# Kernel optimization log

Measured on AMD Instinct MI355X. Metric: run time of the kernel, lower is better.

Reference implementation:

```python
import jax, jax.numpy as jnp
import numpy as np

N = 50000   # nodes
E = 200000  # edges (avg degree ~4, pose-graph-like sparsity)
F_IN = 512
NEG_SLOPE = 0.01  # F.leaky_relu default


def _softmax_aggr(src_feat, dst, num_nodes):
    # torch_geometric SoftmaxAggregation(t=1): per-destination, per-feature
    # alpha = softmax(x_j), out = sum_j alpha * x_j
    m = jax.ops.segment_max(src_feat, dst, num_segments=num_nodes)  # [N,F]
    m = jnp.where(jnp.isfinite(m), m, 0.0)  # empty segments -> -inf guard
    e = jnp.exp(src_feat - m[dst])                                   # [E,F]
    denom = jax.ops.segment_sum(e, dst, num_segments=num_nodes)      # [N,F]
    num = jax.ops.segment_sum(e * src_feat, dst, num_segments=num_nodes)
    return num / jnp.maximum(denom, 1e-16)  # 0 for isolated nodes


def setup_inputs() -> dict:
    key = jax.random.key(0)
    ks = jax.random.split(key, 9)
    inp = {
        "x": jax.random.normal(ks[0], (N, F_IN), dtype=jnp.float32),
        "W1_rel": jax.random.normal(ks[1], (513, 256), dtype=jnp.float32) * 0.04,
        "b1_rel": jnp.zeros((256,), dtype=jnp.float32),
        "W1_root": jax.random.normal(ks[2], (513, 256), dtype=jnp.float32) * 0.04,
        "W2_rel": jax.random.normal(ks[3], (257, 64), dtype=jnp.float32) * 0.06,
        "b2_rel": jnp.zeros((64,), dtype=jnp.float32),
        "W2_root": jax.random.normal(ks[4], (257, 64), dtype=jnp.float32) * 0.06,
        "Wp": jax.random.normal(ks[5], (65, 3), dtype=jnp.float32) * 0.1,
        "bp": jnp.zeros((3,), dtype=jnp.float32),
        "Wr": jax.random.normal(ks[6], (65, 4), dtype=jnp.float32) * 0.1,
        "br": jnp.zeros((4,), dtype=jnp.float32),
        "edge_index": jax.random.randint(ks[7], (2, E), 0, N, dtype=jnp.int64),
    }
    return inp


def reference(x, W1_rel, b1_rel, W1_root, W2_rel, b2_rel, W2_root,
              Wp, bp, Wr, br, edge_index):
    src, dst = edge_index[0], edge_index[1]
    node_index = jnp.arange(x.shape[0], dtype=x.dtype)[:, None]  # [N,1]

    # dropout is identity in eval mode
    h = jnp.concatenate([x, node_index], axis=1)  # [N,513]

    # GraphConv(513,256, aggr='softmax'): lin_rel(softmax_aggr(x_j)) + lin_root(x)
    agg1 = _softmax_aggr(h[src], dst, x.shape[0])               # [N,513]
    h = agg1 @ W1_rel + b1_rel + h @ W1_root                     # [N,256]
    h = jnp.where(h >= 0, h, NEG_SLOPE * h)

    h = jnp.concatenate([h, node_index], axis=1)  # [N,257]

    # GraphConv(257,64) default aggr='add'
    agg2 = jax.ops.segment_sum(h[src], dst, num_segments=x.shape[0])  # [N,257]
    h = agg2 @ W2_rel + b2_rel + h @ W2_root                           # [N,64]
    h = jnp.where(h >= 0, h, NEG_SLOPE * h)

    h = jnp.concatenate([h, node_index], axis=1)  # [N,65]

    position = h @ Wp + bp                         # [N,3]
    rotation = h @ Wr + br                         # [N,4]
    norm = jnp.linalg.norm(rotation, axis=1, keepdims=True)
    rotation = rotation / jnp.maximum(norm, 1e-12)  # F.normalize

    return jnp.concatenate([position, rotation], axis=1)  # [N,7]
```

## Files before the change

### kernel.cpp

```cpp
#include <hip/hip_runtime.h>

#define NNODES 50000
#define NEDGES 200000
#define NSCANB ((NNODES + 255) / 256)

typedef short  bf16x8 __attribute__((ext_vector_type(8)));
typedef float  f32x4  __attribute__((ext_vector_type(4)));
typedef unsigned int u32x4 __attribute__((ext_vector_type(4)));

__device__ __forceinline__ unsigned short f2bf(float f) {
    union { float f; unsigned int u; } c; c.f = f;
    unsigned int r = c.u + 0x7fffu + ((c.u >> 16) & 1u);
    return (unsigned short)(r >> 16);
}
__device__ __forceinline__ float bf2f(unsigned short h) {
    union { unsigned int u; float f; } c; c.u = ((unsigned int)h) << 16;
    return c.f;
}
__device__ __forceinline__ float bflo(unsigned int v) {
    union { unsigned int u; float f; } c; c.u = v << 16;
    return c.f;
}
__device__ __forceinline__ float bfhi(unsigned int v) {
    union { unsigned int u; float f; } c; c.u = v & 0xffff0000u;
    return c.f;
}

#define PREP_B1 (256 * 1024)
#define PREP_B2 (64 * 512)
#define PREP_XC (NNODES * 64)
__global__ __launch_bounds__(256) void k_prepcount(const float* __restrict__ x,
                                                   const float* __restrict__ W1_rel,
                                                   const float* __restrict__ W1_root,
                                                   const float* __restrict__ W2_rel,
                                                   const float* __restrict__ W2_root,
                                                   const int* __restrict__ ei,
                                                   int* __restrict__ deg,
                                                   unsigned short* __restrict__ Bt1,
                                                   unsigned short* __restrict__ Bt2,
                                                   unsigned short* __restrict__ xb) {
    const int gtid = blockIdx.x * 256 + threadIdx.x;
    const int GS = gridDim.x * 256;
    for (int e = gtid; e < NEDGES; e += GS) atomicAdd(&deg[ei[NEDGES + e]], 1);
    for (int i = gtid; i < PREP_B1; i += GS) {
        int n = i >> 10, k = i & 1023;
        float v = (k < 512) ? W1_rel[k * 256 + n] : W1_root[(k - 512) * 256 + n];
        Bt1[i] = f2bf(v);
    }
    for (int i = gtid; i < PREP_B2; i += GS) {
        int n = i >> 9, k = i & 511;
        float v = (k < 256) ? W2_rel[k * 64 + n] : W2_root[(k - 256) * 64 + n];
        Bt2[i] = f2bf(v);
    }
    for (int i = gtid; i < PREP_XC; i += GS) {
        int n = i >> 6, c8 = (i & 63) * 8;
        const float* xp = x + (size_t)n * 512 + c8;
        float4 a = *(const float4*)xp;
        float4 bb = *(const float4*)(xp + 4);
        unsigned short o[8];
        o[0] = f2bf(a.x); o[1] = f2bf(a.y); o[2] = f2bf(a.z); o[3] = f2bf(a.w);
        o[4] = f2bf(bb.x); o[5] = f2bf(bb.y); o[6] = f2bf(bb.z); o[7] = f2bf(bb.w);
        *(u32x4*)(xb + (size_t)n * 512 + c8) = *(const u32x4*)o;
    }
}

__global__ __launch_bounds__(256) void k_scanA(const int* __restrict__ deg,
                                               int* __restrict__ rs,
                                               int* __restrict__ partials) {
    __shared__ int sm[256];
    int t = threadIdx.x, i = blockIdx.x * 256 + t;
    int v = (i < NNODES) ? deg[i] : 0;
    sm[t] = v;
    __syncthreads();
#pragma unroll
    for (int off = 1; off < 256; off <<= 1) {
        int u = (t >= off) ? sm[t - off] : 0;
        __syncthreads();
        sm[t] += u;
        __syncthreads();
    }
    if (i < NNODES) rs[i] = sm[t] - v;
    if (t == 255) partials[blockIdx.x] = sm[255];
}

__global__ __launch_bounds__(256) void k_scanC2(int* __restrict__ rs,
                                                const int* __restrict__ partials,
                                                int* __restrict__ cursor) {
    __shared__ int sm[256];
    int t = threadIdx.x, b = blockIdx.x;
    sm[t] = (t < b && t < NSCANB) ? partials[t] : 0;
    __syncthreads();
#pragma unroll
    for (int off = 128; off; off >>= 1) {
        if (t < off) sm[t] += sm[t + off];
        __syncthreads();
    }
    int off0 = sm[0];
    int i = b * 256 + t;
    if (i < NNODES) {
        int rv = rs[i] + off0;
        rs[i] = rv;
        cursor[i] = rv;
    }
    if (i == 0) rs[NNODES] = NEDGES;
}

__global__ void k_scatter(const int* __restrict__ ei, int* __restrict__ cursor,
                          int* __restrict__ srcs) {
    int e = blockIdx.x * 256 + threadIdx.x;
    if (e < NEDGES) {
        int d = ei[NEDGES + e];
        int p = atomicAdd(&cursor[d], 1);
        srcs[p] = ei[e];
    }
}

__global__ __launch_bounds__(256) void k_agg1(const unsigned short* __restrict__ xb,
                                              const int* __restrict__ rs,
                                              const int* __restrict__ srcs,
                                              unsigned short* __restrict__ AggBuf) {
    int wv = threadIdx.x >> 6;
    int lane = threadIdx.x & 63;
    int n = blockIdx.x * 4 + wv;
    int e0 = rs[n], e1 = rs[n + 1];
    float nu[8], de[8];
#pragma unroll
    for (int j = 0; j < 8; ++j) { nu[j] = 0.f; de[j] = 0.f; }
    int e = e0;
    for (; e + 1 < e1; e += 2) {
        int s0 = srcs[e], s1 = srcs[e + 1];
        u32x4 r0 = *(const u32x4*)(xb + (size_t)s0 * 512 + lane * 8);
        u32x4 r1 = *(const u32x4*)(xb + (size_t)s1 * 512 + lane * 8);
#pragma unroll
        for (int p = 0; p < 4; ++p) {
            float v0 = bflo(r0[p]), v1 = bfhi(r0[p]);
            float E0 = __expf(v0), E1 = __expf(v1);
            de[2 * p] += E0; nu[2 * p] += E0 * v0;
            de[2 * p + 1] += E1; nu[2 * p + 1] += E1 * v1;
        }
#pragma unroll
        for (int p = 0; p < 4; ++p) {
            float v0 = bflo(r1[p]), v1 = bfhi(r1[p]);
            float E0 = __expf(v0), E1 = __expf(v1);
            de[2 * p] += E0; nu[2 * p] += E0 * v0;
            de[2 * p + 1] += E1; nu[2 * p + 1] += E1 * v1;
        }
    }
    if (e < e1) {
        int s0 = srcs[e];
        u32x4 r0 = *(const u32x4*)(xb + (size_t)s0 * 512 + lane * 8);
#pragma unroll
        for (int p = 0; p < 4; ++p) {
            float v0 = bflo(r0[p]), v1 = bfhi(r0[p]);
            float E0 = __expf(v0), E1 = __expf(v1);
            de[2 * p] += E0; nu[2 * p] += E0 * v0;
            de[2 * p + 1] += E1; nu[2 * p + 1] += E1 * v1;
        }
    }
    unsigned short o[8];
#pragma unroll
    for (int j = 0; j < 8; ++j) o[j] = f2bf(nu[j] / fmaxf(de[j], 1e-16f));
    *(u32x4*)(AggBuf + (size_t)n * 512 + lane * 8) = *(const u32x4*)o;
}

__global__ __launch_bounds__(256) void k_agg2(const int* __restrict__ rs,
                                              const int* __restrict__ srcs,
                                              const unsigned short* __restrict__ H1,
                                              unsigned short* __restrict__ Seg) {
    int wv = threadIdx.x >> 6;
    int lane = threadIdx.x & 63;
    int n = blockIdx.x * 4 + wv;
    int e0 = rs[n], e1 = rs[n + 1];
    float a[4] = {0.f, 0.f, 0.f, 0.f};
    int e = e0;
    for (; e + 1 < e1; e += 2) {
        int s0 = srcs[e], s1 = srcs[e + 1];
        uint2 r0 = *(const uint2*)(H1 + (size_t)s0 * 256 + lane * 4);
        uint2 r1 = *(const uint2*)(H1 + (size_t)s1 * 256 + lane * 4);
        a[0] += bflo(r0.x) + bflo(r1.x);
        a[1] += bfhi(r0.x) + bfhi(r1.x);
        a[2] += bflo(r0.y) + bflo(r1.y);
        a[3] += bfhi(r0.y) + bfhi(r1.y);
    }
    if (e < e1) {
        uint2 r0 = *(const uint2*)(H1 + (size_t)srcs[e] * 256 + lane * 4);
        a[0] += bflo(r0.x); a[1] += bfhi(r0.x);
        a[2] += bflo(r0.y); a[3] += bfhi(r0.y);
    }
    uint2 o;
    o.x = (unsigned int)f2bf(a[0]) | ((unsigned int)f2bf(a[1]) << 16);
    o.y = (unsigned int)f2bf(a[2]) | ((unsigned int)f2bf(a[3]) << 16);
    *(uint2*)(Seg + (size_t)n * 256 + lane * 4) = o;
}

__global__ __launch_bounds__(256, 5) void k_gemm1(const unsigned short* __restrict__ A1,
                                                  const unsigned short* __restrict__ A2,
                                                  const unsigned short* __restrict__ Bt,
                                                  const int* __restrict__ rs,
                                                  const int* __restrict__ srcs,
                                                  const float* __restrict__ r1,
                                                  const float* __restrict__ r2,
                                                  const float* __restrict__ bias,
                                                  unsigned short* __restrict__ outp) {
    constexpr int BM = 64, BN = 128, BK = 64;
    __shared__ __align__(16) unsigned short As[BM * BK];
    __shared__ __align__(16) unsigned short Bs[BN * BK];
    __shared__ float s1t[BM];

    const int tid = threadIdx.x;
    const int w = tid >> 6;
    const int lane = tid & 63;
    const int lm = lane & 15;
    const int quad = lane >> 4;
    const int wr = w >> 1;
    const int wc = w & 1;
    const int rowbase = blockIdx.y * BM;
    const int colbase = blockIdx.x * BN;
    const int wrow = wr * 32;
    const int wcol = wc * 64;

    const int rsub = lane >> 3;
    const int csw = (lane & 7) ^ rsub;

    f32x4 acc[2][4];
#pragma unroll
    for (int mi = 0; mi < 2; ++mi)
#pragma unroll
        for (int ni = 0; ni < 4; ++ni) acc[mi][ni] = (f32x4){0.f, 0.f, 0.f, 0.f};

    for (int kt = 0; kt < 1024; kt += BK) {
        const unsigned short* Ab = (kt < 512) ? A1 : A2;
        int kof = (kt < 512) ? kt : kt - 512;
#pragma unroll
        for (int l = 0; l < 2; ++l) {
            int r = w * 16 + l * 8;
            int gr = rowbase + r + rsub;
            if (gr >= NNODES) gr = NNODES - 1;
            const unsigned short* gp = Ab + (size_t)gr * 512 + kof + csw * 8;
            __builtin_amdgcn_global_load_lds(
                (const __attribute__((address_space(1))) void*)gp,
                (__attribute__((address_space(3))) void*)(As + r * BK), 16, 0, 0);
        }
#pragma unroll
        for (int l = 0; l < 4; ++l) {
            int r = w * 32 + l * 8;
            const unsigned short* gp = Bt + (size_t)(colbase + r + rsub) * 1024 + kt + csw * 8;
            __builtin_amdgcn_global_load_lds(
                (const __attribute__((address_space(1))) void*)gp,
                (__attribute__((address_space(3))) void*)(Bs + r * BK), 16, 0, 0);
        }
        __syncthreads();
#pragma unroll
        for (int kk = 0; kk < BK; kk += 32) {
            const int kidx = (kk >> 3) + quad;
            const int phys = kidx ^ (lm & 7);
            bf16x8 af[2], bfr[4];
#pragma unroll
            for (int mi = 0; mi < 2; ++mi)
                af[mi] = __builtin_bit_cast(bf16x8,
                    *(const u32x4*)(As + (wrow + mi * 16 + lm) * BK + phys * 8));
#pragma unroll
            for (int ni = 0; ni < 4; ++ni)
                bfr[ni] = __builtin_bit_cast(bf16x8,
                    *(const u32x4*)(Bs + (wcol + ni * 16 + lm) * BK + phys * 8));
#pragma unroll
            for (int mi = 0; mi < 2; ++mi)
#pragma unroll
                for (int ni = 0; ni < 4; ++ni)
                    acc[mi][ni] = __builtin_amdgcn_mfma_f32_16x16x32_bf16(
                        af[mi], bfr[ni], acc[mi][ni], 0, 0, 0);
        }
        __syncthreads();
    }

    if (tid < BM) {
        int grow = rowbase + tid;
        float r_ = 0.f;
        if (grow < NNODES) {
            int e0 = rs[grow], e1 = rs[grow + 1];
            float m = -INFINITY, d = 0.f, q = 0.f;
            for (int e = e0; e < e1; ++e) {
                float v = (float)srcs[e];
                float nm = fmaxf(m, v);
                float sc = __expf(m - nm), ee = __expf(v - nm);
                d = d * sc + ee;
                q = q * sc + ee * v;
                m = nm;
            }
            r_ = q / fmaxf(d, 1e-16f);
        }
        s1t[tid] = r_;
    }
    __syncthreads();

#pragma unroll
    for (int ni = 0; ni < 4; ++ni) {
        int gc = colbase + wcol + ni * 16 + lm;
        float r1v = r1[gc], r2v = r2[gc], bv = bias[gc];
#pragma unroll
        for (int mi = 0; mi < 2; ++mi) {
#pragma unroll
            for (int r = 0; r < 4; ++r) {
                int lrow = wrow + mi * 16 + quad * 4 + r;
                int grow = rowbase + lrow;
                if (grow < NNODES) {
                    float v = acc[mi][ni][r] + s1t[lrow] * r1v + (float)grow * r2v + bv;
                    v = (v >= 0.f) ? v : 0.01f * v;
                    outp[(size_t)grow * 256 + gc] = f2bf(v);
                }
            }
        }
    }
}

__global__ __launch_bounds__(256) void k_gemm2h(const unsigned short* __restrict__ A1,
                                                const unsigned short* __restrict__ A2,
                                                const unsigned short* __restrict__ Bt,
                                                const int* __restrict__ rs,
                                                const int* __restrict__ srcs,
                                                const float* __restrict__ r1,
                                                const float* __restrict__ r2,
                                                const float* __restrict__ bias,
                                                const float* __restrict__ Wp,
                                                const float* __restrict__ bp,
                                                const float* __restrict__ Wr,
                                                const float* __restrict__ br,
                                                float* __restrict__ out) {
    constexpr int BM = 64, BN = 64, BK = 64;
    __shared__ __align__(16) unsigned short As[BM * BK];
    __shared__ __align__(16) unsigned short Bs[BN * BK];
    __shared__ float h2t[BM * 65];
    __shared__ float s1t[BM];

    const int tid = threadIdx.x;
    const int w = tid >> 6;
    const int lane = tid & 63;
    const int lm = lane & 15;
    const int quad = lane >> 4;
    const int rowbase = blockIdx.x * BM;
    const int wrow = w * 16;

    const int rsub = lane >> 3;
    const int csw = (lane & 7) ^ rsub;

    f32x4 acc[4];
#pragma unroll
    for (int ni = 0; ni < 4; ++ni) acc[ni] = (f32x4){0.f, 0.f, 0.f, 0.f};

    for (int kt = 0; kt < 512; kt += BK) {
        const unsigned short* Ab = (kt < 256) ? A1 : A2;
        int kof = (kt < 256) ? kt : kt - 256;
#pragma unroll
        for (int l = 0; l < 2; ++l) {
            int r = w * 16 + l * 8;
            int gr = rowbase + r + rsub;
            if (gr >= NNODES) gr = NNODES - 1;
            const unsigned short* gp = Ab + (size_t)gr * 256 + kof + csw * 8;
            __builtin_amdgcn_global_load_lds(
                (const __attribute__((address_space(1))) void*)gp,
                (__attribute__((address_space(3))) void*)(As + r * BK), 16, 0, 0);
        }
#pragma unroll
        for (int l = 0; l < 2; ++l) {
            int r = w * 16 + l * 8;
            const unsigned short* gp = Bt + (size_t)(r + rsub) * 512 + kt + csw * 8;
            __builtin_amdgcn_global_load_lds(
                (const __attribute__((address_space(1))) void*)gp,
                (__attribute__((address_space(3))) void*)(Bs + r * BK), 16, 0, 0);
        }
        __syncthreads();
#pragma unroll
        for (int kk = 0; kk < BK; kk += 32) {
            const int kidx = (kk >> 3) + quad;
            const int phys = kidx ^ (lm & 7);
            bf16x8 af;
            af = __builtin_bit_cast(bf16x8,
                *(const u32x4*)(As + (wrow + lm) * BK + phys * 8));
            bf16x8 bfr[4];
#pragma unroll
            for (int ni = 0; ni < 4; ++ni)
                bfr[ni] = __builtin_bit_cast(bf16x8,
                    *(const u32x4*)(Bs + (ni * 16 + lm) * BK + phys * 8));
#pragma unroll
            for (int ni = 0; ni < 4; ++ni)
                acc[ni] = __builtin_amdgcn_mfma_f32_16x16x32_bf16(
                    af, bfr[ni], acc[ni], 0, 0, 0);
        }
        __syncthreads();
    }

    if (tid < BM) {
        int grow = rowbase + tid;
        float si = 0.f;
        if (grow < NNODES) {
            int e0 = rs[grow], e1 = rs[grow + 1];
            for (int e = e0; e < e1; ++e) si += (float)srcs[e];
        }
        s1t[tid] = si;
    }
    __syncthreads();

#pragma unroll
    for (int ni = 0; ni < 4; ++ni) {
        int gc = ni * 16 + lm;
        float r1v = r1[gc], r2v = r2[gc], bv = bias[gc];
#pragma unroll
        for (int r = 0; r < 4; ++r) {
            int lrow = wrow + quad * 4 + r;
            int grow = rowbase + lrow;
            float v = acc[ni][r] + s1t[lrow] * r1v + (float)grow * r2v + bv;
            v = (v >= 0.f) ? v : 0.01f * v;
            h2t[lrow * 65 + gc] = v;
        }
    }
    __syncthreads();

    if (tid < BM) {
        int grow = rowbase + tid;
        if (grow < NNODES) {
            const float* hv = h2t + tid * 65;
            float idx = (float)grow;
            float p0 = 0.f, p1 = 0.f, p2 = 0.f;
            float r0 = 0.f, r1a = 0.f, r2a = 0.f, r3 = 0.f;
#pragma unroll 8
            for (int c = 0; c < 64; ++c) {
                float v = hv[c];
                p0 += v * Wp[c * 3 + 0];
                p1 += v * Wp[c * 3 + 1];
                p2 += v * Wp[c * 3 + 2];
                r0 += v * Wr[c * 4 + 0];
                r1a += v * Wr[c * 4 + 1];
                r2a += v * Wr[c * 4 + 2];
                r3 += v * Wr[c * 4 + 3];
            }
            p0 += idx * Wp[64 * 3 + 0] + bp[0];
            p1 += idx * Wp[64 * 3 + 1] + bp[1];
            p2 += idx * Wp[64 * 3 + 2] + bp[2];
            r0 += idx * Wr[64 * 4 + 0] + br[0];
            r1a += idx * Wr[64 * 4 + 1] + br[1];
            r2a += idx * Wr[64 * 4 + 2] + br[2];
            r3 += idx * Wr[64 * 4 + 3] + br[3];
            float nrm = fmaxf(sqrtf(r0 * r0 + r1a * r1a + r2a * r2a + r3 * r3), 1e-12f);
            float* op = out + (size_t)grow * 7;
            op[0] = p0; op[1] = p1; op[2] = p2;
            op[3] = r0 / nrm; op[4] = r1a / nrm; op[5] = r2a / nrm; op[6] = r3 / nrm;
        }
    }
}

extern "C" void kernel_launch(void* const* d_in, const int* in_sizes, int n_in,
                              void* d_out, int out_size, void* d_ws, size_t ws_size,
                              hipStream_t stream) {
    const float* x       = (const float*)d_in[0];
    const float* W1_rel  = (const float*)d_in[1];
    const float* b1      = (const float*)d_in[2];
    const float* W1_root = (const float*)d_in[3];
    const float* W2_rel  = (const float*)d_in[4];
    const float* b2      = (const float*)d_in[5];
    const float* W2_root = (const float*)d_in[6];
    const float* Wp      = (const float*)d_in[7];
    const float* bp      = (const float*)d_in[8];
    const float* Wr      = (const float*)d_in[9];
    const float* br      = (const float*)d_in[10];
    const int*   ei      = (const int*)d_in[11];
    float* out = (float*)d_out;

    char* ws = (char*)d_ws;
    size_t off = 0;
    auto alloc = [&](size_t bytes) {
        size_t o = off;
        off = (off + bytes + 255) & ~(size_t)255;
        return (void*)(ws + o);
    };
    int*   deg       = (int*)alloc(NNODES * 4);
    int*   cursor    = (int*)alloc(NNODES * 4);
    int*   row_start = (int*)alloc((NNODES + 1) * 4);
    int*   srcs      = (int*)alloc(NEDGES * 4);
    int*   partials  = (int*)alloc(NSCANB * 4);
    unsigned short* xb     = (unsigned short*)alloc((size_t)NNODES * 512 * 2);
    unsigned short* AggBuf = (unsigned short*)alloc((size_t)NNODES * 512 * 2);
    unsigned short* H1     = (unsigned short*)alloc((size_t)NNODES * 256 * 2);
    unsigned short* Seg    = (unsigned short*)alloc((size_t)NNODES * 256 * 2);
    unsigned short* Bt1    = (unsigned short*)alloc(256 * 1024 * 2);
    unsigned short* Bt2    = (unsigned short*)alloc(64 * 512 * 2);

    hipMemsetAsync(deg, 0, NNODES * 4, stream);

    k_prepcount<<<2048, 256, 0, stream>>>(
        x, W1_rel, W1_root, W2_rel, W2_root, ei, deg, Bt1, Bt2, xb);

    k_scanA<<<NSCANB, 256, 0, stream>>>(deg, row_start, partials);
    k_scanC2<<<NSCANB, 256, 0, stream>>>(row_start, partials, cursor);
    k_scatter<<<(NEDGES + 255) / 256, 256, 0, stream>>>(ei, cursor, srcs);

    k_agg1<<<NNODES / 4, 256, 0, stream>>>(xb, row_start, srcs, AggBuf);

    k_gemm1<<<dim3(2, (NNODES + 63) / 64), 256, 0, stream>>>(
        AggBuf, xb, Bt1, row_start, srcs, W1_rel + 512 * 256, W1_root + 512 * 256, b1, H1);

    k_agg2<<<NNODES / 4, 256, 0, stream>>>(row_start, srcs, H1, Seg);

    k_gemm2h<<<(NNODES + 63) / 64, 256, 0, stream>>>(
        Seg, H1, Bt2, row_start, srcs, W2_rel + 256 * 64, W2_root + 256 * 64, b2,
        Wp, bp, Wr, br, out);
}
```

Measured before the change: 341.1 us.

## Double-buffer LDS tiles in both GEMM kernels to overlap loads with MFMA

Both GEMM kernels now keep two LDS buffers for the A and B tiles. The next K-tile is issued via global_load_lds while the current tile is consumed, using partial vmcnt waits and raw s_barrier calls. The aim is to hide global-to-LDS latency behind MFMA work rather than serialising load then compute. In exchange, LDS usage per block doubles, which can lower occupancy (gemm1 declares 5 blocks per CU), and the hand-counted vmcnt values must match the number of outstanding loads per stage.

```diff
diff --git a/kernel.cpp b/kernel.cpp
--- a/kernel.cpp
+++ b/kernel.cpp
@@ -203,8 +203,8 @@
                                                   const float* __restrict__ bias,
                                                   unsigned short* __restrict__ outp) {
     constexpr int BM = 64, BN = 128, BK = 64;
-    __shared__ __align__(16) unsigned short As[BM * BK];
-    __shared__ __align__(16) unsigned short Bs[BN * BK];
+    __shared__ __align__(16) unsigned short As[2][BM * BK];
+    __shared__ __align__(16) unsigned short Bs[2][BN * BK];
     __shared__ float s1t[BM];
 
     const int tid = threadIdx.x;
@@ -228,7 +228,7 @@
 #pragma unroll
         for (int ni = 0; ni < 4; ++ni) acc[mi][ni] = (f32x4){0.f, 0.f, 0.f, 0.f};
 
-    for (int kt = 0; kt < 1024; kt += BK) {
+    auto stage = [&](unsigned short* Asb, unsigned short* Bsb, int kt) {
         const unsigned short* Ab = (kt < 512) ? A1 : A2;
         int kof = (kt < 512) ? kt : kt - 512;
 #pragma unroll
@@ -239,7 +239,7 @@
             const unsigned short* gp = Ab + (size_t)gr * 512 + kof + csw * 8;
             __builtin_amdgcn_global_load_lds(
                 (const __attribute__((address_space(1))) void*)gp,
-                (__attribute__((address_space(3))) void*)(As + r * BK), 16, 0, 0);
+                (__attribute__((address_space(3))) void*)(Asb + r * BK), 16, 0, 0);
         }
 #pragma unroll
         for (int l = 0; l < 4; ++l) {
@@ -247,9 +247,11 @@
             const unsigned short* gp = Bt + (size_t)(colbase + r + rsub) * 1024 + kt + csw * 8;
             __builtin_amdgcn_global_load_lds(
                 (const __attribute__((address_space(1))) void*)gp,
-                (__attribute__((address_space(3))) void*)(Bs + r * BK), 16, 0, 0);
-        }
-        __syncthreads();
+                (__attribute__((address_space(3))) void*)(Bsb + r * BK), 16, 0, 0);
+        }
+    };
+
+    auto compute = [&](const unsigned short* Asb, const unsigned short* Bsb) {
 #pragma unroll
         for (int kk = 0; kk < BK; kk += 32) {
             const int kidx = (kk >> 3) + quad;
@@ -258,11 +260,11 @@
 #pragma unroll
             for (int mi = 0; mi < 2; ++mi)
                 af[mi] = __builtin_bit_cast(bf16x8,
-                    *(const u32x4*)(As + (wrow + mi * 16 + lm) * BK + phys * 8));
+                    *(const u32x4*)(Asb + (wrow + mi * 16 + lm) * BK + phys * 8));
 #pragma unroll
             for (int ni = 0; ni < 4; ++ni)
                 bfr[ni] = __builtin_bit_cast(bf16x8,
-                    *(const u32x4*)(Bs + (wcol + ni * 16 + lm) * BK + phys * 8));
+                    *(const u32x4*)(Bsb + (wcol + ni * 16 + lm) * BK + phys * 8));
 #pragma unroll
             for (int mi = 0; mi < 2; ++mi)
 #pragma unroll
@@ -270,7 +272,27 @@
                     acc[mi][ni] = __builtin_amdgcn_mfma_f32_16x16x32_bf16(
                         af[mi], bfr[ni], acc[mi][ni], 0, 0, 0);
         }
-        __syncthreads();
+    };
+
+    stage(As[0], Bs[0], 0);
+#pragma unroll 1
+    for (int t = 0; t < 16; t += 2) {
+        stage(As[1], Bs[1], (t + 1) * BK);
+        asm volatile("s_waitcnt vmcnt(6)" ::: "memory");
+        __builtin_amdgcn_s_barrier();
+        __builtin_amdgcn_sched_barrier(0);
+        compute(As[0], Bs[0]);
+        __builtin_amdgcn_s_barrier();
+        if (t + 2 < 16) {
+            stage(As[0], Bs[0], (t + 2) * BK);
+            asm volatile("s_waitcnt vmcnt(6)" ::: "memory");
+        } else {
+            asm volatile("s_waitcnt vmcnt(0)" ::: "memory");
+        }
+        __builtin_amdgcn_s_barrier();
+        __builtin_amdgcn_sched_barrier(0);
+        compute(As[1], Bs[1]);
+        __builtin_amdgcn_s_barrier();
     }
 
     if (tid < BM) {
@@ -327,8 +349,8 @@
                                                 const float* __restrict__ br,
                                                 float* __restrict__ out) {
     constexpr int BM = 64, BN = 64, BK = 64;
-    __shared__ __align__(16) unsigned short As[BM * BK];
-    __shared__ __align__(16) unsigned short Bs[BN * BK];
+    __shared__ __align__(16) unsigned short As[2][BM * BK];
+    __shared__ __align__(16) unsigned short Bs[2][BN * BK];
     __shared__ float h2t[BM * 65];
     __shared__ float s1t[BM];
 
@@ -347,7 +369,7 @@
 #pragma unroll
     for (int ni = 0; ni < 4; ++ni) acc[ni] = (f32x4){0.f, 0.f, 0.f, 0.f};
 
-    for (int kt = 0; kt < 512; kt += BK) {
+    auto stage = [&](unsigned short* Asb, unsigned short* Bsb, int kt) {
         const unsigned short* Ab = (kt < 256) ? A1 : A2;
         int kof = (kt < 256) ? kt : kt - 256;
 #pragma unroll
@@ -358,7 +380,7 @@
             const unsigned short* gp = Ab + (size_t)gr * 256 + kof + csw * 8;
             __builtin_amdgcn_global_load_lds(
                 (const __attribute__((address_space(1))) void*)gp,
-                (__attribute__((address_space(3))) void*)(As + r * BK), 16, 0, 0);
+                (__attribute__((address_space(3))) void*)(Asb + r * BK), 16, 0, 0);
         }
 #pragma unroll
         for (int l = 0; l < 2; ++l) {
@@ -366,27 +388,49 @@
             const unsigned short* gp = Bt + (size_t)(r + rsub) * 512 + kt + csw * 8;
             __builtin_amdgcn_global_load_lds(
                 (const __attribute__((address_space(1))) void*)gp,
-                (__attribute__((address_space(3))) void*)(Bs + r * BK), 16, 0, 0);
-        }
-        __syncthreads();
+                (__attribute__((address_space(3))) void*)(Bsb + r * BK), 16, 0, 0);
+        }
+    };
+
+    auto compute = [&](const unsigned short* Asb, const unsigned short* Bsb) {
 #pragma unroll
         for (int kk = 0; kk < BK; kk += 32) {
             const int kidx = (kk >> 3) + quad;
             const int phys = kidx ^ (lm & 7);
             bf16x8 af;
             af = __builtin_bit_cast(bf16x8,
-                *(const u32x4*)(As + (wrow + lm) * BK + phys * 8));
+                *(const u32x4*)(Asb + (wrow + lm) * BK + phys * 8));
             bf16x8 bfr[4];
 #pragma unroll
             for (int ni = 0; ni < 4; ++ni)
                 bfr[ni] = __builtin_bit_cast(bf16x8,
-                    *(const u32x4*)(Bs + (ni * 16 + lm) * BK + phys * 8));
+                    *(const u32x4*)(Bsb + (ni * 16 + lm) * BK + phys * 8));
 #pragma unroll
             for (int ni = 0; ni < 4; ++ni)
                 acc[ni] = __builtin_amdgcn_mfma_f32_16x16x32_bf16(
                     af, bfr[ni], acc[ni], 0, 0, 0);
         }
-        __syncthreads();
+    };
+
+    stage(As[0], Bs[0], 0);
+#pragma unroll 1
+    for (int t = 0; t < 8; t += 2) {
+        stage(As[1], Bs[1], (t + 1) * BK);
+        asm volatile("s_waitcnt vmcnt(4)" ::: "memory");
+        __builtin_amdgcn_s_barrier();
+        __builtin_amdgcn_sched_barrier(0);
+        compute(As[0], Bs[0]);
+        __builtin_amdgcn_s_barrier();
+        if (t + 2 < 8) {
+            stage(As[0], Bs[0], (t + 2) * BK);
+            asm volatile("s_waitcnt vmcnt(4)" ::: "memory");
+        } else {
+            asm volatile("s_waitcnt vmcnt(0)" ::: "memory");
+        }
+        __builtin_amdgcn_s_barrier();
+        __builtin_amdgcn_sched_barrier(0);
+        compute(As[1], Bs[1]);
+        __builtin_amdgcn_s_barrier();
     }
 
     if (tid < BM) {
```

Measured after the change: 353.7 us. 3.7% more time.

## Fuse softmax and sum neighbor aggregations into the GEMM A-tile producers

Applied to the files above, without the earlier changes.

Removes the separate aggregation kernels and their intermediate buffers. Each GEMM now computes the aggregated A tile on the fly from CSR neighbor lists and writes it into shared memory. GEMM1 widens to a 512-thread block covering all 256 output columns, so each row's aggregation is done once rather than per column block. This saves the global write and read of the aggregate buffers, but it serializes the irregular gather latency inside the GEMM K-loop and drops the asynchronous A loads for the aggregated half.

```diff
diff --git a/kernel.cpp b/kernel.cpp
--- a/kernel.cpp
+++ b/kernel.cpp
@@ -12,10 +12,6 @@
     union { float f; unsigned int u; } c; c.f = f;
     unsigned int r = c.u + 0x7fffu + ((c.u >> 16) & 1u);
     return (unsigned short)(r >> 16);
-}
-__device__ __forceinline__ float bf2f(unsigned short h) {
-    union { unsigned int u; float f; } c; c.u = ((unsigned int)h) << 16;
-    return c.f;
 }
 __device__ __forceinline__ float bflo(unsigned int v) {
     union { unsigned int u; float f; } c; c.u = v << 16;
@@ -115,94 +111,15 @@
     }
 }
 
-__global__ __launch_bounds__(256) void k_agg1(const unsigned short* __restrict__ xb,
-                                              const int* __restrict__ rs,
-                                              const int* __restrict__ srcs,
-                                              unsigned short* __restrict__ AggBuf) {
-    int wv = threadIdx.x >> 6;
-    int lane = threadIdx.x & 63;
-    int n = blockIdx.x * 4 + wv;
-    int e0 = rs[n], e1 = rs[n + 1];
-    float nu[8], de[8];
-#pragma unroll
-    for (int j = 0; j < 8; ++j) { nu[j] = 0.f; de[j] = 0.f; }
-    int e = e0;
-    for (; e + 1 < e1; e += 2) {
-        int s0 = srcs[e], s1 = srcs[e + 1];
-        u32x4 r0 = *(const u32x4*)(xb + (size_t)s0 * 512 + lane * 8);
-        u32x4 r1 = *(const u32x4*)(xb + (size_t)s1 * 512 + lane * 8);
-#pragma unroll
-        for (int p = 0; p < 4; ++p) {
-            float v0 = bflo(r0[p]), v1 = bfhi(r0[p]);
-            float E0 = __expf(v0), E1 = __expf(v1);
-            de[2 * p] += E0; nu[2 * p] += E0 * v0;
-            de[2 * p + 1] += E1; nu[2 * p + 1] += E1 * v1;
-        }
-#pragma unroll
-        for (int p = 0; p < 4; ++p) {
-            float v0 = bflo(r1[p]), v1 = bfhi(r1[p]);
-            float E0 = __expf(v0), E1 = __expf(v1);
-            de[2 * p] += E0; nu[2 * p] += E0 * v0;
-            de[2 * p + 1] += E1; nu[2 * p + 1] += E1 * v1;
-        }
-    }
-    if (e < e1) {
-        int s0 = srcs[e];
-        u32x4 r0 = *(const u32x4*)(xb + (size_t)s0 * 512 + lane * 8);
-#pragma unroll
-        for (int p = 0; p < 4; ++p) {
-            float v0 = bflo(r0[p]), v1 = bfhi(r0[p]);
-            float E0 = __expf(v0), E1 = __expf(v1);
-            de[2 * p] += E0; nu[2 * p] += E0 * v0;
-            de[2 * p + 1] += E1; nu[2 * p + 1] += E1 * v1;
-        }
-    }
-    unsigned short o[8];
-#pragma unroll
-    for (int j = 0; j < 8; ++j) o[j] = f2bf(nu[j] / fmaxf(de[j], 1e-16f));
-    *(u32x4*)(AggBuf + (size_t)n * 512 + lane * 8) = *(const u32x4*)o;
-}
-
-__global__ __launch_bounds__(256) void k_agg2(const int* __restrict__ rs,
-                                              const int* __restrict__ srcs,
-                                              const unsigned short* __restrict__ H1,
-                                              unsigned short* __restrict__ Seg) {
-    int wv = threadIdx.x >> 6;
-    int lane = threadIdx.x & 63;
-    int n = blockIdx.x * 4 + wv;
-    int e0 = rs[n], e1 = rs[n + 1];
-    float a[4] = {0.f, 0.f, 0.f, 0.f};
-    int e = e0;
-    for (; e + 1 < e1; e += 2) {
-        int s0 = srcs[e], s1 = srcs[e + 1];
-        uint2 r0 = *(const uint2*)(H1 + (size_t)s0 * 256 + lane * 4);
-        uint2 r1 = *(const uint2*)(H1 + (size_t)s1 * 256 + lane * 4);
-        a[0] += bflo(r0.x) + bflo(r1.x);
-        a[1] += bfhi(r0.x) + bfhi(r1.x);
-        a[2] += bflo(r0.y) + bflo(r1.y);
-        a[3] += bfhi(r0.y) + bfhi(r1.y);
-    }
-    if (e < e1) {
-        uint2 r0 = *(const uint2*)(H1 + (size_t)srcs[e] * 256 + lane * 4);
-        a[0] += bflo(r0.x); a[1] += bfhi(r0.x);
-        a[2] += bflo(r0.y); a[3] += bfhi(r0.y);
-    }
-    uint2 o;
-    o.x = (unsigned int)f2bf(a[0]) | ((unsigned int)f2bf(a[1]) << 16);
-    o.y = (unsigned int)f2bf(a[2]) | ((unsigned int)f2bf(a[3]) << 16);
-    *(uint2*)(Seg + (size_t)n * 256 + lane * 4) = o;
-}
-
-__global__ __launch_bounds__(256, 5) void k_gemm1(const unsigned short* __restrict__ A1,
-                                                  const unsigned short* __restrict__ A2,
-                                                  const unsigned short* __restrict__ Bt,
-                                                  const int* __restrict__ rs,
-                                                  const int* __restrict__ srcs,
-                                                  const float* __restrict__ r1,
-                                                  const float* __restrict__ r2,
-                                                  const float* __restrict__ bias,
-                                                  unsigned short* __restrict__ outp) {
-    constexpr int BM = 64, BN = 128, BK = 64;
+__global__ __launch_bounds__(512) void k_gemm1f(const unsigned short* __restrict__ xb,
+                                                const unsigned short* __restrict__ Bt,
+                                                const int* __restrict__ rs,
+                                                const int* __restrict__ srcs,
+                                                const float* __restrict__ r1,
+                                                const float* __restrict__ r2,
+                                                const float* __restrict__ bias,
+                                                unsigned short* __restrict__ outp) {
+    constexpr int BM = 64, BN = 256, BK = 64;
     __shared__ __align__(16) unsigned short As[BM * BK];
     __shared__ __align__(16) unsigned short Bs[BN * BK];
     __shared__ float s1t[BM];
@@ -212,42 +129,81 @@
     const int lane = tid & 63;
     const int lm = lane & 15;
     const int quad = lane >> 4;
-    const int wr = w >> 1;
-    const int wc = w & 1;
-    const int rowbase = blockIdx.y * BM;
-    const int colbase = blockIdx.x * BN;
+    const int wr = w >> 2;
+    const int wc = w & 3;
+    const int rowbase = blockIdx.x * BM;
     const int wrow = wr * 32;
     const int wcol = wc * 64;
-
     const int rsub = lane >> 3;
     const int csw = (lane & 7) ^ rsub;
 
+    const int arow = w * 8 + rsub;
+    const int acb = lane & 7;
+    int g_arow = rowbase + arow;
+    if (g_arow >= NNODES) g_arow = NNODES - 1;
+    const int ae0 = rs[g_arow], ae1 = rs[g_arow + 1];
+
     f32x4 acc[2][4];
 #pragma unroll
     for (int mi = 0; mi < 2; ++mi)
 #pragma unroll
         for (int ni = 0; ni < 4; ++ni) acc[mi][ni] = (f32x4){0.f, 0.f, 0.f, 0.f};
 
+#pragma unroll 1
     for (int kt = 0; kt < 1024; kt += BK) {
-        const unsigned short* Ab = (kt < 512) ? A1 : A2;
-        int kof = (kt < 512) ? kt : kt - 512;
-#pragma unroll
-        for (int l = 0; l < 2; ++l) {
-            int r = w * 16 + l * 8;
-            int gr = rowbase + r + rsub;
-            if (gr >= NNODES) gr = NNODES - 1;
-            const unsigned short* gp = Ab + (size_t)gr * 512 + kof + csw * 8;
-            __builtin_amdgcn_global_load_lds(
-                (const __attribute__((address_space(1))) void*)gp,
-                (__attribute__((address_space(3))) void*)(As + r * BK), 16, 0, 0);
-        }
 #pragma unroll
         for (int l = 0; l < 4; ++l) {
             int r = w * 32 + l * 8;
-            const unsigned short* gp = Bt + (size_t)(colbase + r + rsub) * 1024 + kt + csw * 8;
+            const unsigned short* gp = Bt + (size_t)(r + rsub) * 1024 + kt + csw * 8;
             __builtin_amdgcn_global_load_lds(
                 (const __attribute__((address_space(1))) void*)gp,
                 (__attribute__((address_space(3))) void*)(Bs + r * BK), 16, 0, 0);
+        }
+        if (kt < 512) {
+            float nu[8], de[8];
+#pragma unroll
+            for (int j = 0; j < 8; ++j) { nu[j] = 0.f; de[j] = 0.f; }
+            const unsigned short* xrow = xb + kt + acb * 8;
+            int e = ae0;
+            for (; e + 1 < ae1; e += 2) {
+                int s0 = srcs[e], s1 = srcs[e + 1];
+                u32x4 q0 = *(const u32x4*)(xrow + (size_t)s0 * 512);
+                u32x4 q1 = *(const u32x4*)(xrow + (size_t)s1 * 512);
+#pragma unroll
+                for (int p = 0; p < 4; ++p) {
+                    float v0 = bflo(q0[p]), v1 = bfhi(q0[p]);
+                    float E0 = __expf(v0), E1 = __expf(v1);
+                    de[2 * p] += E0; nu[2 * p] += E0 * v0;
+                    de[2 * p + 1] += E1; nu[2 * p + 1] += E1 * v1;
+                }
+#pragma unroll
+                for (int p = 0; p < 4; ++p) {
+                    float v0 = bflo(q1[p]), v1 = bfhi(q1[p]);
+                    float E0 = __expf(v0), E1 = __expf(v1);
+                    de[2 * p] += E0; nu[2 * p] += E0 * v0;
+                    de[2 * p + 1] += E1; nu[2 * p + 1] += E1 * v1;
+                }
+            }
+            if (e < ae1) {
+                int s0 = srcs[e];
+                u32x4 q0 = *(const u32x4*)(xrow + (size_t)s0 * 512);
+#pragma unroll
+                for (int p = 0; p < 4; ++p) {
+                    float v0 = bflo(q0[p]), v1 = bfhi(q0[p]);
+                    float E0 = __expf(v0), E1 = __expf(v1);
+                    de[2 * p] += E0; nu[2 * p] += E0 * v0;
+                    de[2 * p + 1] += E1; nu[2 * p + 1] += E1 * v1;
+                }
+            }
+            unsigned short o[8];
+#pragma unroll
+            for (int j = 0; j < 8; ++j) o[j] = f2bf(nu[j] / fmaxf(de[j], 1e-16f));
+            *(u32x4*)(As + arow * BK + csw * 8) = *(const u32x4*)o;
+        } else {
+            const unsigned short* gp = xb + (size_t)g_arow * 512 + (kt - 512) + csw * 8;
+            __builtin_amdgcn_global_load_lds(
+                (const __attribute__((address_space(1))) void*)gp,
+                (__attribute__((address_space(3))) void*)(As + (w * 8) * BK), 16, 0, 0);
         }
         __syncthreads();
 #pragma unroll
@@ -295,7 +251,7 @@
 
 #pragma unroll
     for (int ni = 0; ni < 4; ++ni) {
-        int gc = colbase + wcol + ni * 16 + lm;
+        int gc = wcol + ni * 16 + lm;
         float r1v = r1[gc], r2v = r2[gc], bv = bias[gc];
 #pragma unroll
         for (int mi = 0; mi < 2; ++mi) {
@@ -313,19 +269,18 @@
     }
 }
 
-__global__ __launch_bounds__(256) void k_gemm2h(const unsigned short* __restrict__ A1,
-                                                const unsigned short* __restrict__ A2,
-                                                const unsigned short* __restrict__ Bt,
-                                                const int* __restrict__ rs,
-                                                const int* __restrict__ srcs,
-                                                const float* __restrict__ r1,
-                                                const float* __restrict__ r2,
-                                                const float* __restrict__ bias,
-                                                const float* __restrict__ Wp,
-                                                const float* __restrict__ bp,
-                                                const float* __restrict__ Wr,
-                                                const float* __restrict__ br,
-                                                float* __restrict__ out) {
+__global__ __launch_bounds__(256) void k_gemm2hf(const unsigned short* __restrict__ H1,
+                                                 const unsigned short* __restrict__ Bt,
+                                                 const int* __restrict__ rs,
+                                                 const int* __restrict__ srcs,
+                                                 const float* __restrict__ r1,
+                                                 const float* __restrict__ r2,
+                                                 const float* __restrict__ bias,
+                                                 const float* __restrict__ Wp,
+                                                 const float* __restrict__ bp,
+                                                 const float* __restrict__ Wr,
+                                                 const float* __restrict__ br,
+                                                 float* __restrict__ out) {
     constexpr int BM = 64, BN = 64, BK = 64;
     __shared__ __align__(16) unsigned short As[BM * BK];
     __shared__ __align__(16) unsigned short Bs[BN * BK];
@@ -339,27 +294,23 @@
     const int quad = lane >> 4;
     const int rowbase = blockIdx.x * BM;
     const int wrow = w * 16;
-
     const int rsub = lane >> 3;
     const int csw = (lane & 7) ^ rsub;
 
+    const int ar0 = w * 8 + rsub;
+    const int ar1 = 32 + w * 8 + rsub;
+    const int acb = lane & 7;
+    int g0 = rowbase + ar0; if (g0 >= NNODES) g0 = NNODES - 1;
+    int g1 = rowbase + ar1; if (g1 >= NNODES) g1 = NNODES - 1;
+    const int e00 = rs[g0], e01 = rs[g0 + 1];
+    const int e10 = rs[g1], e11 = rs[g1 + 1];
+
     f32x4 acc[4];
 #pragma unroll
     for (int ni = 0; ni < 4; ++ni) acc[ni] = (f32x4){0.f, 0.f, 0.f, 0.f};
 
+#pragma unroll 1
     for (int kt = 0; kt < 512; kt += BK) {
-        const unsigned short* Ab = (kt < 256) ? A1 : A2;
-        int kof = (kt < 256) ? kt : kt - 256;
-#pragma unroll
-        for (int l = 0; l < 2; ++l) {
-            int r = w * 16 + l * 8;
-            int gr = rowbase + r + rsub;
-            if (gr >= NNODES) gr = NNODES - 1;
-            const unsigned short* gp = Ab + (size_t)gr * 256 + kof + csw * 8;
-            __builtin_amdgcn_global_load_lds(
-                (const __attribute__((address_space(1))) void*)gp,
-                (__attribute__((address_space(3))) void*)(As + r * BK), 16, 0, 0);
-        }
 #pragma unroll
         for (int l = 0; l < 2; ++l) {
             int r = w * 16 + l * 8;
@@ -367,6 +318,51 @@
             __builtin_amdgcn_global_load_lds(
                 (const __attribute__((address_space(1))) void*)gp,
                 (__attribute__((address_space(3))) void*)(Bs + r * BK), 16, 0, 0);
+        }
+        if (kt < 256) {
+            const unsigned short* hrow = H1 + kt + acb * 8;
+#pragma unroll
+            for (int pass = 0; pass < 2; ++pass) {
+                int ar = pass ? ar1 : ar0;
+                int e = pass ? e10 : e00;
+                int eend = pass ? e11 : e01;
+                float a[8];
+#pragma unroll
+                for (int j = 0; j < 8; ++j) a[j] = 0.f;
+                for (; e + 1 < eend; e += 2) {
+                    int s0 = srcs[e], s1 = srcs[e + 1];
+                    u32x4 q0 = *(const u32x4*)(hrow + (size_t)s0 * 256);
+                    u32x4 q1 = *(const u32x4*)(hrow + (size_t)s1 * 256);
+#pragma unroll
+                    for (int p = 0; p < 4; ++p) {
+                        a[2 * p] += bflo(q0[p]) + bflo(q1[p]);
+                        a[2 * p + 1] += bfhi(q0[p]) + bfhi(q1[p]);
+                    }
+                }
+                if (e < eend) {
+                    u32x4 q0 = *(const u32x4*)(hrow + (size_t)srcs[e] * 256);
+#pragma unroll
+                    for (int p = 0; p < 4; ++p) {
+                        a[2 * p] += bflo(q0[p]);
+                        a[2 * p + 1] += bfhi(q0[p]);
+                    }
+                }
+                unsigned short o[8];
+#pragma unroll
+                for (int j = 0; j < 8; ++j) o[j] = f2bf(a[j]);
+                *(u32x4*)(As + ar * BK + csw * 8) = *(const u32x4*)o;
+            }
+        } else {
+#pragma unroll
+            for (int l = 0; l < 2; ++l) {
+                int r = w * 16 + l * 8;
+                int gr = rowbase + r + rsub;
+                if (gr >= NNODES) gr = NNODES - 1;
+                const unsigned short* gp = H1 + (size_t)gr * 256 + (kt - 256) + csw * 8;
+                __builtin_amdgcn_global_load_lds(
+                    (const __attribute__((address_space(1))) void*)gp,
+                    (__attribute__((address_space(3))) void*)(As + r * BK), 16, 0, 0);
+            }
         }
         __syncthreads();
 #pragma unroll
@@ -478,9 +474,7 @@
     int*   srcs      = (int*)alloc(NEDGES * 4);
     int*   partials  = (int*)alloc(NSCANB * 4);
     unsigned short* xb     = (unsigned short*)alloc((size_t)NNODES * 512 * 2);
-    unsigned short* AggBuf = (unsigned short*)alloc((size_t)NNODES * 512 * 2);
     unsigned short* H1     = (unsigned short*)alloc((size_t)NNODES * 256 * 2);
-    unsigned short* Seg    = (unsigned short*)alloc((size_t)NNODES * 256 * 2);
     unsigned short* Bt1    = (unsigned short*)alloc(256 * 1024 * 2);
     unsigned short* Bt2    = (unsigned short*)alloc(64 * 512 * 2);
 
@@ -493,14 +487,10 @@
     k_scanC2<<<NSCANB, 256, 0, stream>>>(row_start, partials, cursor);
     k_scatter<<<(NEDGES + 255) / 256, 256, 0, stream>>>(ei, cursor, srcs);
 
-    k_agg1<<<NNODES / 4, 256, 0, stream>>>(xb, row_start, srcs, AggBuf);
-
-    k_gemm1<<<dim3(2, (NNODES + 63) / 64), 256, 0, stream>>>(
-        AggBuf, xb, Bt1, row_start, srcs, W1_rel + 512 * 256, W1_root + 512 * 256, b1, H1);
-
-    k_agg2<<<NNODES / 4, 256, 0, stream>>>(row_start, srcs, H1, Seg);
-
-    k_gemm2h<<<(NNODES + 63) / 64, 256, 0, stream>>>(
-        Seg, H1, Bt2, row_start, srcs, W2_rel + 256 * 64, W2_root + 256 * 64, b2,
+    k_gemm1f<<<(NNODES + 63) / 64, 512, 0, stream>>>(
+        xb, Bt1, row_start, srcs, W1_rel + 512 * 256, W1_root + 512 * 256, b1, H1);
+
+    k_gemm2hf<<<(NNODES + 63) / 64, 256, 0, stream>>>(
+        H1, Bt2, row_start, srcs, W2_rel + 256 * 64, W2_root + 256 * 64, b2,
         Wp, bp, Wr, br, out);
 }
```

New measurement: 378.0 us. 10.8% more time.
